# Optimization experiments

Hardware: AMD Instinct MI355X
Metric: run time of the kernel (lower is better)

## Reference

```python
import jax, jax.numpy as jnp
import numpy as np

# config constants
B, L, ENC_IN = 8, 512, 7
D_MODEL = 768
EXPAND = 2
D_INNER = D_MODEL * EXPAND          # 1536
DT_RANK = (D_MODEL + 15) // 16      # 48
N_STATE = 16                         # configs.d_ff acts as SSM state size
K_CONV = 4
E_LAYERS = 2
C_OUT = 7
PRED_LEN = 96
EPS = 1e-5


def rmsnorm(x, w):
    return x * jax.lax.rsqrt(jnp.mean(x * x, axis=-1, keepdims=True) + EPS) * w


def silu(x):
    return x * jax.nn.sigmoid(x)


def positional_embedding(l, d):
    pos = np.arange(l, dtype=np.float32)[:, None]
    div = np.exp(np.arange(0, d, 2, dtype=np.float32) * (-np.log(10000.0) / d))
    pe = np.zeros((l, d), dtype=np.float32)
    pe[:, 0::2] = np.sin(pos * div)
    pe[:, 1::2] = np.cos(pos * div)
    return jnp.asarray(pe)


def causal_dwconv(x, w, b):
    # x: [b, d, l], w: [d, 1, k]; torch pads k-1 both sides then slices [:l] == left-pad k-1
    y = jax.lax.conv_general_dilated(
        x, w, window_strides=(1,), padding=[(K_CONV - 1, 0)],
        dimension_numbers=('NCH', 'OIH', 'NCH'), feature_group_count=D_INNER)
    return y + b[None, :, None]


def selective_scan(u, delta, A, Bm, Cm, Dp):
    # u, delta: [b,l,d]; A: [d,n]; Bm, Cm: [b,l,n]; Dp: [d]
    deltaA = jnp.exp(jnp.einsum('bld,dn->bldn', delta, A))          # [b,l,d,n]
    deltaBu = (delta * u)[..., None] * Bm[:, :, None, :]             # [b,l,d,n]

    def step(xc, inp):
        dA, dBu, Ct = inp                                            # [b,d,n],[b,d,n],[b,n]
        xc = dA * xc + dBu
        return xc, jnp.einsum('bdn,bn->bd', xc, Ct)

    b, l, d = u.shape
    x0 = jnp.zeros((b, d, A.shape[1]), u.dtype)
    _, ys = jax.lax.scan(step, x0, (jnp.moveaxis(deltaA, 1, 0),
                                    jnp.moveaxis(deltaBu, 1, 0),
                                    jnp.moveaxis(Cm, 1, 0)))
    y = jnp.moveaxis(ys, 0, 1)                                       # [b,l,d]
    return y + u * Dp


def mamba_block(x, in_w, conv_w, conv_b, xproj_w, dtproj_w, dtproj_b, A_log, Dp, outproj_w):
    xr = x @ in_w.T                                                  # [b,l,2*d_inner]
    xs, res = xr[..., :D_INNER], xr[..., D_INNER:]
    xs = causal_dwconv(jnp.swapaxes(xs, 1, 2), conv_w, conv_b)
    xs = silu(jnp.swapaxes(xs, 1, 2))
    # ssm
    A = -jnp.exp(A_log)
    x_dbl = xs @ xproj_w.T                                           # [b,l,dt_rank+2n]
    delta = x_dbl[..., :DT_RANK]
    Bm = x_dbl[..., DT_RANK:DT_RANK + N_STATE]
    Cm = x_dbl[..., DT_RANK + N_STATE:]
    delta = jax.nn.softplus(delta @ dtproj_w.T + dtproj_b)
    y = selective_scan(xs, delta, A, Bm, Cm, Dp)
    y = y * silu(res)
    return y @ outproj_w.T


def setup_inputs() -> dict:
    key = jax.random.key(0)
    ks = iter(jax.random.split(key, 32))
    s = 0.02
    d = {}
    d['x'] = jax.random.normal(next(ks), (B, L, ENC_IN), jnp.float32)
    d['token_w'] = jax.random.normal(next(ks), (D_MODEL, ENC_IN, 3), jnp.float32) * s
    d['time_w'] = jax.random.normal(next(ks), (D_MODEL, 1), jnp.float32) * s
    d['norm_w'] = jnp.ones((E_LAYERS, D_MODEL), jnp.float32)
    d['in_w'] = jax.random.normal(next(ks), (E_LAYERS, 2 * D_INNER, D_MODEL), jnp.float32) * s
    d['conv_w'] = jax.random.normal(next(ks), (E_LAYERS, D_INNER, 1, K_CONV), jnp.float32) * s
    d['conv_b'] = jnp.zeros((E_LAYERS, D_INNER), jnp.float32)
    d['xproj_w'] = jax.random.normal(next(ks), (E_LAYERS, DT_RANK + 2 * N_STATE, D_INNER), jnp.float32) * s
    d['dtproj_w'] = jax.random.normal(next(ks), (E_LAYERS, D_INNER, DT_RANK), jnp.float32) * s
    d['dtproj_b'] = jnp.zeros((E_LAYERS, D_INNER), jnp.float32)
    A = np.tile(np.arange(1, N_STATE + 1, dtype=np.float32)[None, :], (D_INNER, 1))
    d['A_log'] = jnp.tile(jnp.log(jnp.asarray(A))[None], (E_LAYERS, 1, 1))
    d['Dp'] = jnp.ones((E_LAYERS, D_INNER), jnp.float32)
    d['outproj_w'] = jax.random.normal(next(ks), (E_LAYERS, D_MODEL, D_INNER), jnp.float32) * s
    d['final_norm_w'] = jnp.ones((D_MODEL,), jnp.float32)
    d['out_w'] = jax.random.normal(next(ks), (C_OUT, D_MODEL), jnp.float32) * s
    return d


def reference(x, token_w, time_w, norm_w, in_w, conv_w, conv_b, xproj_w,
              dtproj_w, dtproj_b, A_log, Dp, outproj_w, final_norm_w, out_w):
    # instance normalization (mean/std detached)
    mean_enc = jax.lax.stop_gradient(jnp.mean(x, axis=1, keepdims=True))
    xc = x - mean_enc
    std_enc = jax.lax.stop_gradient(jnp.sqrt(jnp.var(xc, axis=1, keepdims=True) + 1e-5))
    xc = xc / std_enc
    # DataEmbedding: circular conv token emb + sinusoidal pos + timeF linear
    xp = jnp.pad(jnp.swapaxes(xc, 1, 2), ((0, 0), (0, 0), (1, 1)), mode='wrap')
    tok = jax.lax.conv_general_dilated(xp, token_w, (1,), 'VALID',
                                       dimension_numbers=('NCH', 'OIH', 'NCH'))
    tok = jnp.swapaxes(tok, 1, 2)                                    # [b,l,d_model]
    x_mark = (jnp.arange(L, dtype=x.dtype) / L)[None, :, None]       # [1,l,1]
    h = tok + positional_embedding(L, D_MODEL)[None] + x_mark @ time_w.T
    for e in range(E_LAYERS):
        h = mamba_block(rmsnorm(h, norm_w[e]), in_w[e], conv_w[e], conv_b[e],
                        xproj_w[e], dtproj_w[e], dtproj_b[e], A_log[e], Dp[e],
                        outproj_w[e]) + h
    h = rmsnorm(h, final_norm_w)
    out = h @ out_w.T
    out = out * std_enc + mean_enc
    return out[:, -PRED_LEN:, :]
```

## Files before the change

### kernel.cpp

```cpp
#include <hip/hip_runtime.h>
#include <hip/hip_bf16.h>
#include <math.h>

#define BSZ 8
#define LSEQ 512
#define ENC_IN 7
#define D_MODEL 768
#define D_INNER 1536
#define DT_RANK 48
#define N_STATE 16
#define K_CONV 4
#define E_LAYERS 2
#define C_OUT 7
#define PRED_LEN 96
#define EPSV 1e-5f
#define XN 80
#define KSPLIT 4

#define ROWS (BSZ*LSEQ)
#define NC 16
#define CL (LSEQ/NC)
#define NTILE (LSEQ/16)
#define LOG2E 1.44269504088896f

typedef __bf16 bf16x8 __attribute__((ext_vector_type(8)));
typedef float  f32x4  __attribute__((ext_vector_type(4)));

__device__ __forceinline__ float fexp2(float x) {
    float r;
    asm("v_exp_f32 %0, %1" : "=v"(r) : "v"(x));
    return r;
}
__device__ __forceinline__ float softplusf(float v) {
    return fmaxf(v, 0.f) + log1pf(__expf(-fabsf(v)));
}
__device__ __forceinline__ void glds16(const char* g, char* l) {
    __builtin_amdgcn_global_load_lds((const __attribute__((address_space(1))) unsigned int*)g,
                                     (__attribute__((address_space(3))) unsigned int*)l, 16, 0, 0);
}

__device__ __forceinline__ float block_sum(float v, float* tmp) {
    #pragma unroll
    for (int off = 32; off > 0; off >>= 1) v += __shfl_down(v, off);
    int lane = threadIdx.x & 63, wid = threadIdx.x >> 6;
    __syncthreads();
    if (lane == 0) tmp[wid] = v;
    __syncthreads();
    return tmp[0] + tmp[1] + tmp[2] + tmp[3];
}

__global__ __launch_bounds__(256) void cvt_all(const float* __restrict__ in_w,
                                               const float* __restrict__ outw,
                                               const float* __restrict__ xpw,
                                               const float* __restrict__ dtw,
                                               __hip_bfloat16* __restrict__ inw_bf,
                                               __hip_bfloat16* __restrict__ outw_bf,
                                               __hip_bfloat16* __restrict__ xpw_bf,
                                               __hip_bfloat16* __restrict__ dtw_bf) {
    const int N1 = E_LAYERS*2*D_INNER*D_MODEL;
    const int N2 = E_LAYERS*D_MODEL*D_INNER;
    const int N3 = E_LAYERS*XN*D_INNER;
    const int N4 = E_LAYERS*D_INNER*64;
    int i = blockIdx.x*256 + threadIdx.x;
    if (i < N1) {
        inw_bf[i] = __float2bfloat16(in_w[i]);
    } else if (i < N1+N2) {
        int j = i - N1; outw_bf[j] = __float2bfloat16(outw[j]);
    } else if (i < N1+N2+N3) {
        int j = i - N1 - N2; xpw_bf[j] = __float2bfloat16(xpw[j]);
    } else if (i < N1+N2+N3+N4) {
        int j = i - N1 - N2 - N3;
        int r = j >> 6, c = j & 63;
        dtw_bf[j] = __float2bfloat16(c < DT_RANK ? dtw[r*DT_RANK + c] : 0.f);
    }
}

__global__ __launch_bounds__(256) void stats_kernel(const float* __restrict__ x,
                                                    float* __restrict__ mean,
                                                    float* __restrict__ stdv) {
    int bc = blockIdx.x;
    int b = bc / ENC_IN, c = bc % ENC_IN;
    __shared__ float tmp[4];
    float s = 0.f, sq = 0.f;
    for (int l = threadIdx.x; l < LSEQ; l += 256) {
        float v = x[((size_t)(b*LSEQ + l))*ENC_IN + c];
        s += v; sq += v*v;
    }
    s = block_sum(s, tmp);
    sq = block_sum(sq, tmp);
    if (threadIdx.x == 0) {
        float m = s / LSEQ;
        float var = sq / LSEQ - m*m;
        if (var < 0.f) var = 0.f;
        mean[bc] = m;
        stdv[bc] = sqrtf(var + EPSV);
    }
}

__global__ __launch_bounds__(256) void embed_kernel(const float* __restrict__ x,
                                                    const float* __restrict__ token_w,
                                                    const float* __restrict__ time_w,
                                                    const float* __restrict__ mean,
                                                    const float* __restrict__ stdv,
                                                    float* __restrict__ h) {
    int bl = blockIdx.x;
    int b = bl >> 9, l = bl & 511;
    __shared__ float sxc[ENC_IN*3];
    if (threadIdx.x < ENC_IN*3) {
        int c = threadIdx.x / 3, k = threadIdx.x % 3;
        int lk = (l + k - 1) & 511;
        float v = x[((size_t)(b*LSEQ + lk))*ENC_IN + c];
        sxc[threadIdx.x] = (v - mean[b*ENC_IN + c]) / stdv[b*ENC_IN + c];
    }
    __syncthreads();
    #pragma unroll
    for (int i = 0; i < 3; i++) {
        int d = threadIdx.x + i*256;
        float acc = 0.f;
        const float* w = token_w + (size_t)d*21;
        #pragma unroll
        for (int t = 0; t < 21; t++) acc += sxc[t] * w[t];
        int d2 = d & ~1;
        float div = __expf((float)d2 * (-9.210340371976184f / (float)D_MODEL));
        float ang = (float)l * div;
        float pe = (d & 1) ? cosf(ang) : sinf(ang);
        float tm = ((float)l / (float)LSEQ) * time_w[d];
        h[(size_t)bl*D_MODEL + d] = acc + pe + tm;
    }
}

__global__ __launch_bounds__(256) void rmsnorm_bf16(const float* __restrict__ h,
                                                    const float* __restrict__ w,
                                                    __hip_bfloat16* __restrict__ xn) {
    size_t base = (size_t)blockIdx.x * D_MODEL;
    __shared__ float tmp[4];
    float ss = 0.f;
    for (int k = threadIdx.x; k < D_MODEL; k += 256) { float v = h[base+k]; ss += v*v; }
    ss = block_sum(ss, tmp);
    float inv = rsqrtf(ss / (float)D_MODEL + EPSV);
    for (int k = threadIdx.x; k < D_MODEL; k += 256)
        xn[base+k] = __float2bfloat16(h[base+k]*inv*w[k]);
}

__global__ __launch_bounds__(256) void gemm_inproj(const __hip_bfloat16* __restrict__ A,
                                                   const __hip_bfloat16* __restrict__ Bw,
                                                   __hip_bfloat16* __restrict__ Cxs,
                                                   __hip_bfloat16* __restrict__ Cg) {
    __shared__ __align__(16) __hip_bfloat16 As[2][128*32];
    __shared__ __align__(16) __hip_bfloat16 Bs[2][128*32];
    const int K = D_MODEL;
    int tid = threadIdx.x, lane = tid & 63, w = tid >> 6;
    int gx = gridDim.x;
    int nwg = gx * gridDim.y;
    int orig = blockIdx.y*gx + blockIdx.x;
    int swz = (orig & 7)*(nwg >> 3) + (orig >> 3);
    int m0 = (swz / gx) * 128, n0 = (swz % gx) * 128;
    int wr = w >> 1, wc = w & 1;
    int kq = lane >> 4, rr = lane & 15;

    f32x4 acc[4][4];
    #pragma unroll
    for (int i = 0; i < 4; i++)
        #pragma unroll
        for (int j = 0; j < 4; j++) acc[i][j] = (f32x4){0.f,0.f,0.f,0.f};

    const char* Ab = (const char*)A;
    const char* Bb = (const char*)Bw;
    char* AsB = (char*)As;
    char* BsB = (char*)Bs;

    int c0 = tid, c1 = tid + 256;
    int r0 = c0 >> 2, q0 = (c0 & 3) ^ ((r0 >> 1) & 3);
    int r1 = c1 >> 2, q1 = (c1 & 3) ^ ((r1 >> 1) & 3);
    int sw = (kq ^ ((rr >> 1) & 3)) * 16;

    glds16(Ab + ((size_t)(m0+r0)*K + 0 + q0*8)*2, AsB + c0*16);
    glds16(Ab + ((size_t)(m0+r1)*K + 0 + q1*8)*2, AsB + c1*16);
    glds16(Bb + ((size_t)(n0+r0)*K + 0 + q0*8)*2, BsB + c0*16);
    glds16(Bb + ((size_t)(n0+r1)*K + 0 + q1*8)*2, BsB + c1*16);
    asm volatile("s_waitcnt vmcnt(0)" ::: "memory");
    __syncthreads();

    int cur = 0;
    for (int k0 = 0; k0 < K; k0 += 32) {
        if (k0 + 32 < K) {
            int nb = cur ^ 1;
            glds16(Ab + ((size_t)(m0+r0)*K + k0+32 + q0*8)*2, AsB + nb*8192 + c0*16);
            glds16(Ab + ((size_t)(m0+r1)*K + k0+32 + q1*8)*2, AsB + nb*8192 + c1*16);
            glds16(Bb + ((size_t)(n0+r0)*K + k0+32 + q0*8)*2, BsB + nb*8192 + c0*16);
            glds16(Bb + ((size_t)(n0+r1)*K + k0+32 + q1*8)*2, BsB + nb*8192 + c1*16);
        }
        bf16x8 af[4], bfr[4];
        #pragma unroll
        for (int mi = 0; mi < 4; mi++) af[mi]  = *(const bf16x8*)(AsB + cur*8192 + (wr*64 + mi*16 + rr)*64 + sw);
        #pragma unroll
        for (int ni = 0; ni < 4; ni++) bfr[ni] = *(const bf16x8*)(BsB + cur*8192 + (wc*64 + ni*16 + rr)*64 + sw);
        #pragma unroll
        for (int mi = 0; mi < 4; mi++)
            #pragma unroll
            for (int ni = 0; ni < 4; ni++)
                acc[mi][ni] = __builtin_amdgcn_mfma_f32_16x16x32_bf16(af[mi], bfr[ni], acc[mi][ni], 0, 0, 0);
        asm volatile("s_waitcnt vmcnt(0)" ::: "memory");
        __syncthreads();
        cur ^= 1;
    }

    #pragma unroll
    for (int mi = 0; mi < 4; mi++) {
        #pragma unroll
        for (int ni = 0; ni < 4; ni++) {
            int row0 = m0 + wr*64 + mi*16;
            int col  = n0 + wc*64 + ni*16 + rr;
            if (col >= D_INNER) {
                __hip_bfloat16 g4[4];
                #pragma unroll
                for (int r = 0; r < 4; r++) {
                    float v = acc[mi][ni][r];
                    g4[r] = __float2bfloat16(v / (1.f + __expf(-v)));
                }
                int cd = col - D_INNER;
                *(uint2*)&Cg[((size_t)(row0 >> 4)*D_INNER + cd)*16 + kq*4] = *(uint2*)g4;
            } else {
                #pragma unroll
                for (int r = 0; r < 4; r++) {
                    int row = row0 + kq*4 + r;
                    Cxs[(size_t)row*D_INNER + col] = __float2bfloat16(acc[mi][ni][r]);
                }
            }
        }
    }
}

__global__ __launch_bounds__(256) void gemm_dtproj(const __hip_bfloat16* __restrict__ A,
                                                   const __hip_bfloat16* __restrict__ Bw,
                                                   const float* __restrict__ bias,
                                                   __hip_bfloat16* __restrict__ C) {
    __shared__ __align__(16) __hip_bfloat16 As[128*64];
    __shared__ __align__(16) __hip_bfloat16 Bs[128*64];
    const int K = 64;
    int tid = threadIdx.x, lane = tid & 63, w = tid >> 6;
    int gx = gridDim.x;
    int nwg = gx * gridDim.y;
    int orig = blockIdx.y*gx + blockIdx.x;
    int swz = (orig & 7)*(nwg >> 3) + (orig >> 3);
    int m0 = (swz / gx) * 128, n0 = (swz % gx) * 128;
    int wr = w >> 1, wc = w & 1;
    int kq = lane >> 4, rr = lane & 15;

    f32x4 acc[4][4];
    #pragma unroll
    for (int i = 0; i < 4; i++)
        #pragma unroll
        for (int j = 0; j < 4; j++) acc[i][j] = (f32x4){0.f,0.f,0.f,0.f};

    const char* Ab = (const char*)A;
    const char* Bb = (const char*)Bw;
    char* AsB = (char*)As;
    char* BsB = (char*)Bs;

    #pragma unroll
    for (int c = 0; c < 4; c++) {
        int idx = c*256 + tid;
        int r = idx >> 3, q = idx & 7;
        int qs = q ^ (r & 7);
        glds16(Ab + ((size_t)(m0+r)*K + qs*8)*2, AsB + idx*16);
        glds16(Bb + ((size_t)(n0+r)*K + qs*8)*2, BsB + idx*16);
    }
    __syncthreads();

    #pragma unroll
    for (int kh = 0; kh < 2; kh++) {
        int ch = ((kh*4 + kq) ^ (rr & 7)) * 16;
        bf16x8 af[4], bfr[4];
        #pragma unroll
        for (int mi = 0; mi < 4; mi++) af[mi]  = *(const bf16x8*)(AsB + (wr*64 + mi*16 + rr)*128 + ch);
        #pragma unroll
        for (int ni = 0; ni < 4; ni++) bfr[ni] = *(const bf16x8*)(BsB + (wc*64 + ni*16 + rr)*128 + ch);
        #pragma unroll
        for (int mi = 0; mi < 4; mi++)
            #pragma unroll
            for (int ni = 0; ni < 4; ni++)
                acc[mi][ni] = __builtin_amdgcn_mfma_f32_16x16x32_bf16(af[mi], bfr[ni], acc[mi][ni], 0, 0, 0);
    }

    #pragma unroll
    for (int mi = 0; mi < 4; mi++) {
        #pragma unroll
        for (int ni = 0; ni < 4; ni++) {
            int row0 = m0 + wr*64 + mi*16;
            int col  = n0 + wc*64 + ni*16 + rr;
            __hip_bfloat16 d4[4];
            #pragma unroll
            for (int r = 0; r < 4; r++) {
                float v = acc[mi][ni][r] + bias[col];
                d4[r] = __float2bfloat16(softplusf(v));
            }
            *(uint2*)&C[((size_t)(row0 >> 4)*D_INNER + col)*16 + kq*4] = *(uint2*)d4;
        }
    }
}

__global__ __launch_bounds__(256) void gemm_outproj(const __hip_bfloat16* __restrict__ A,
                                                    const __hip_bfloat16* __restrict__ Bw,
                                                    float* __restrict__ C) {
    __shared__ __align__(16) __hip_bfloat16 As[2][128*32];
    __shared__ __align__(16) __hip_bfloat16 Bs[2][64*32];
    int tid = threadIdx.x, lane = tid & 63, w = tid >> 6;
    int gx = gridDim.x;
    int nwg = gx * gridDim.y;
    int orig = blockIdx.y*gx + blockIdx.x;
    int swz = (orig & 7)*(nwg >> 3) + (orig >> 3);
    int m0 = (swz / gx) * 128, n0 = (swz % gx) * 64;
    int wr = w >> 1, wc = w & 1;
    int kq = lane >> 4, rr = lane & 15;
    const int K = D_INNER;

    f32x4 acc[4][2];
    #pragma unroll
    for (int i = 0; i < 4; i++)
        #pragma unroll
        for (int j = 0; j < 2; j++) acc[i][j] = (f32x4){0.f,0.f,0.f,0.f};

    const char* Ab = (const char*)A;
    const char* Bb = (const char*)Bw;
    char* AsB = (char*)As;
    char* BsB = (char*)Bs;

    int cA0 = tid, cA1 = tid + 256;
    int rA0 = cA0 >> 2, qA0 = (cA0 & 3) ^ ((rA0 >> 1) & 3);
    int rA1 = cA1 >> 2, qA1 = (cA1 & 3) ^ ((rA1 >> 1) & 3);
    int rB = tid >> 2,  qB  = (tid & 3) ^ ((rB >> 1) & 3);
    int sw = (kq ^ ((rr >> 1) & 3)) * 16;

    glds16(Ab + ((size_t)(m0+rA0)*K + 0 + qA0*8)*2, AsB + cA0*16);
    glds16(Ab + ((size_t)(m0+rA1)*K + 0 + qA1*8)*2, AsB + cA1*16);
    glds16(Bb + ((size_t)(n0+rB)*K + 0 + qB*8)*2, BsB + tid*16);
    asm volatile("s_waitcnt vmcnt(0)" ::: "memory");
    __syncthreads();

    int cur = 0;
    for (int k0 = 0; k0 < K; k0 += 32) {
        if (k0 + 32 < K) {
            int nb = cur ^ 1;
            glds16(Ab + ((size_t)(m0+rA0)*K + k0+32 + qA0*8)*2, AsB + nb*8192 + cA0*16);
            glds16(Ab + ((size_t)(m0+rA1)*K + k0+32 + qA1*8)*2, AsB + nb*8192 + cA1*16);
            glds16(Bb + ((size_t)(n0+rB)*K + k0+32 + qB*8)*2, BsB + nb*4096 + tid*16);
        }
        bf16x8 af[4], bfr[2];
        #pragma unroll
        for (int mi = 0; mi < 4; mi++) af[mi]  = *(const bf16x8*)(AsB + cur*8192 + (wr*64 + mi*16 + rr)*64 + sw);
        #pragma unroll
        for (int ni = 0; ni < 2; ni++) bfr[ni] = *(const bf16x8*)(BsB + cur*4096 + (wc*32 + ni*16 + rr)*64 + sw);
        #pragma unroll
        for (int mi = 0; mi < 4; mi++)
            #pragma unroll
            for (int ni = 0; ni < 2; ni++)
                acc[mi][ni] = __builtin_amdgcn_mfma_f32_16x16x32_bf16(af[mi], bfr[ni], acc[mi][ni], 0, 0, 0);
        asm volatile("s_waitcnt vmcnt(0)" ::: "memory");
        __syncthreads();
        cur ^= 1;
    }

    #pragma unroll
    for (int mi = 0; mi < 4; mi++) {
        #pragma unroll
        for (int ni = 0; ni < 2; ni++) {
            #pragma unroll
            for (int r = 0; r < 4; r++) {
                int row = m0 + wr*64 + mi*16 + kq*4 + r;
                int col = n0 + wc*32 + ni*16 + rr;
                size_t o = (size_t)row*D_MODEL + col;
                C[o] = acc[mi][ni][r] + C[o];
            }
        }
    }
}

__global__ __launch_bounds__(256) void gemm_xproj(const __hip_bfloat16* __restrict__ A,
                                                  const __hip_bfloat16* __restrict__ W,
                                                  float* __restrict__ P) {
    __shared__ __align__(16) __hip_bfloat16 As[2][64*64];
    __shared__ __align__(16) __hip_bfloat16 Bs[2][96*64];
    int tid = threadIdx.x, lane = tid & 63, w = tid >> 6;
    int m0 = blockIdx.x * 64;
    int k0 = blockIdx.y * (D_INNER / KSPLIT);
    int kq = lane >> 4, rr = lane & 15;
    f32x4 acc[5];
    #pragma unroll
    for (int i = 0; i < 5; i++) acc[i] = (f32x4){0.f,0.f,0.f,0.f};
    const char* Ab = (const char*)A;
    const char* Wb = (const char*)W;
    char* AsB = (char*)As;
    char* BsB = (char*)Bs;

    auto stageA = [&](int buf, int kk) {
        #pragma unroll
        for (int cA = 0; cA < 2; cA++) {
            int idx = cA*256 + tid;
            int r = idx >> 3, q = (idx & 7) ^ (r & 7);
            glds16(Ab + ((size_t)(m0+r)*D_INNER + kk + q*8)*2, AsB + buf*8192 + idx*16);
        }
        #pragma unroll
        for (int cB = 0; cB < 3; cB++) {
            int idx = cB*256 + tid;
            int r = idx >> 3, q = (idx & 7) ^ (r & 7);
            int rs = r < XN ? r : XN-1;
            glds16(Wb + ((size_t)rs*D_INNER + kk + q*8)*2, BsB + buf*12288 + idx*16);
        }
    };

    stageA(0, k0);
    asm volatile("s_waitcnt vmcnt(0)" ::: "memory");
    __syncthreads();

    int cur = 0;
    const int kend = k0 + D_INNER/KSPLIT;
    for (int kk = k0; kk < kend; kk += 64) {
        if (kk + 64 < kend) stageA(cur ^ 1, kk + 64);
        #pragma unroll
        for (int kh = 0; kh < 2; kh++) {
            bf16x8 a = *(const bf16x8*)(AsB + cur*8192 + (w*16 + rr)*128 + (((kh*4 + kq) ^ (rr & 7)))*16);
            #pragma unroll
            for (int ni = 0; ni < 5; ni++) {
                bf16x8 b = *(const bf16x8*)(BsB + cur*12288 + (ni*16 + rr)*128 + (((kh*4 + kq) ^ (rr & 7)))*16);
                acc[ni] = __builtin_amdgcn_mfma_f32_16x16x32_bf16(a, b, acc[ni], 0, 0, 0);
            }
        }
        asm volatile("s_waitcnt vmcnt(0)" ::: "memory");
        __syncthreads();
        cur ^= 1;
    }
    float* Cp = P + (size_t)blockIdx.y * ROWS * XN;
    #pragma unroll
    for (int ni = 0; ni < 5; ni++)
        #pragma unroll
        for (int r = 0; r < 4; r++) {
            int row = m0 + w*16 + kq*4 + r;
            int col = ni*16 + rr;
            Cp[(size_t)row*XN + col] = acc[ni][r];
        }
}

__global__ __launch_bounds__(256) void xproj_reduce(const float* __restrict__ P,
                                                    float* __restrict__ xdbl,
                                                    __hip_bfloat16* __restrict__ xdbl_bf) {
    int idx = blockIdx.x*256 + threadIdx.x;
    int col = idx % 96, row = idx / 96;
    if (row >= ROWS) return;
    const size_t RX = (size_t)ROWS*XN;
    if (col < XN) {
        size_t o = (size_t)row*XN + col;
        float s = P[o] + P[RX + o] + P[2*RX + o] + P[3*RX + o];
        xdbl[o] = s;
        if (col < DT_RANK) xdbl_bf[(size_t)row*64 + col] = __float2bfloat16(s);
    } else {
        xdbl_bf[(size_t)row*64 + col - 32] = __float2bfloat16(0.f);
    }
}

__global__ __launch_bounds__(256) void dwconv_silu(const __hip_bfloat16* __restrict__ xs,
                                                   const float* __restrict__ cw,
                                                   const float* __restrict__ cb,
                                                   __hip_bfloat16* __restrict__ u_bf) {
    int idx = blockIdx.x*256 + threadIdx.x;
    int dg = idx % (D_INNER/8);
    int t  = idx / (D_INNER/8);
    if (t >= ROWS) return;
    int d0 = dg*8;
    int l = t & 511, b = t >> 9;
    bf16x8 rows[K_CONV];
    #pragma unroll
    for (int k = 0; k < K_CONV; k++) {
        int ll = l - (K_CONV-1) + k;
        if (ll >= 0) rows[k] = *(const bf16x8*)(xs + ((size_t)(b*LSEQ + ll))*D_INNER + d0);
        else { bf16x8 z = {}; rows[k] = z; }
    }
    bf16x8 outv;
    #pragma unroll
    for (int j = 0; j < 8; j++) {
        int d = d0 + j;
        const float4 w4 = *(const float4*)(cw + d*K_CONV);
        float acc = cb[d]
                  + (float)rows[0][j]*w4.x + (float)rows[1][j]*w4.y
                  + (float)rows[2][j]*w4.z + (float)rows[3][j]*w4.w;
        float v = acc / (1.f + __expf(-acc));
        outv[j] = (__bf16)v;
    }
    *(bf16x8*)(u_bf + (size_t)t*D_INNER + d0) = outv;
}

__global__ __launch_bounds__(256) void scan_p1(const __hip_bfloat16* __restrict__ u,
                                               const __hip_bfloat16* __restrict__ delta_blk,
                                               const float* __restrict__ xdbl,
                                               const float* __restrict__ A_log,
                                               float* __restrict__ xfin,
                                               float* __restrict__ sumdlt) {
    int d = blockIdx.x*256 + threadIdx.x;
    int c = blockIdx.y, b = blockIdx.z;
    int l0 = c*CL;
    const float* al = A_log + d*N_STATE;
    bool fast = true;
    #pragma unroll
    for (int n = 0; n < N_STATE; n++)
        fast = fast && (fabsf(__expf(al[n]) - (float)(n+1)) < 1e-3f);
    float xs[N_STATE];
    #pragma unroll
    for (int n = 0; n < N_STATE; n++) xs[n] = 0.f;
    const __hip_bfloat16* pu = u + (size_t)(b*LSEQ + l0)*D_INNER + d;
    const float* pB = xdbl + (size_t)(b*LSEQ + l0)*XN + DT_RANK;
    float sd = 0.f;
    if (fast) {
        #pragma unroll
        for (int tt = 0; tt < 2; tt++) {
            const __hip_bfloat16* db = delta_blk + ((size_t)(b*NTILE + (l0>>4) + tt)*D_INNER + d)*16;
            bf16x8 d0 = *(const bf16x8*)db;
            bf16x8 d1 = *(const bf16x8*)(db + 8);
            #pragma unroll
            for (int i = 0; i < 16; i++) {
                float dlt = (float)(i < 8 ? d0[i] : d1[i-8]);
                float uu = __bfloat162float(*pu); pu += D_INNER;
                float du = dlt*uu;
                sd += dlt;
                float e1 = fexp2(-dlt*LOG2E);
                float e = e1;
                xs[0] = e*xs[0] + du*pB[0];
                #pragma unroll
                for (int n = 1; n < N_STATE; n++) {
                    e *= e1;
                    xs[n] = e*xs[n] + du*pB[n];
                }
                pB += XN;
            }
        }
    } else {
        #pragma unroll
        for (int tt = 0; tt < 2; tt++) {
            const __hip_bfloat16* db = delta_blk + ((size_t)(b*NTILE + (l0>>4) + tt)*D_INNER + d)*16;
            bf16x8 d0 = *(const bf16x8*)db;
            bf16x8 d1 = *(const bf16x8*)(db + 8);
            #pragma unroll
            for (int i = 0; i < 16; i++) {
                float dlt = (float)(i < 8 ? d0[i] : d1[i-8]);
                float uu = __bfloat162float(*pu); pu += D_INNER;
                float du = dlt*uu;
                sd += dlt;
                #pragma unroll
                for (int n = 0; n < N_STATE; n++) {
                    float A2n = -__expf(al[n]) * LOG2E;
                    xs[n] = fexp2(dlt*A2n)*xs[n] + du*pB[n];
                }
                pB += XN;
            }
        }
    }
    float* px = xfin + (size_t)((b*NC + c)*N_STATE)*D_INNER + d;
    #pragma unroll
    for (int n = 0; n < N_STATE; n++) px[n*D_INNER] = xs[n];
    sumdlt[(size_t)(b*NC + c)*D_INNER + d] = sd;
}

__global__ __launch_bounds__(256) void scan_p2(float* __restrict__ xfin,
                                               const float* __restrict__ sumdlt,
                                               const float* __restrict__ A_log) {
    int idx = blockIdx.x*256 + threadIdx.x;
    int d = idx % D_INNER;
    int r = idx / D_INNER;
    int n = r & 15;
    int b = r >> 4;
    float A2 = -__expf(A_log[d*N_STATE + n]) * LOG2E;
    float cr = 0.f;
    for (int c = 1; c < NC; c++) {
        size_t jp = (size_t)(b*NC + c - 1);
        float xf = xfin[(jp*N_STATE + n)*D_INNER + d];
        float s  = sumdlt[jp*D_INNER + d];
        cr = fexp2(A2 * s) * cr + xf;
        xfin[(jp*N_STATE + n)*D_INNER + d] = cr;
    }
}

__global__ __launch_bounds__(256) void scan_p3(const __hip_bfloat16* __restrict__ u,
                                               const __hip_bfloat16* __restrict__ delta_blk,
                                               const __hip_bfloat16* __restrict__ gres,
                                               const float* __restrict__ xdbl,
                                               const float* __restrict__ A_log,
                                               const float* __restrict__ Dp,
                                               const float* __restrict__ carry,
                                               __hip_bfloat16* __restrict__ ygate) {
    int d = blockIdx.x*256 + threadIdx.x;
    int c = blockIdx.y, b = blockIdx.z;
    int l0 = c*CL;
    const float* al = A_log + d*N_STATE;
    bool fast = true;
    #pragma unroll
    for (int n = 0; n < N_STATE; n++)
        fast = fast && (fabsf(__expf(al[n]) - (float)(n+1)) < 1e-3f);
    float xs[N_STATE];
    if (c == 0) {
        #pragma unroll
        for (int n = 0; n < N_STATE; n++) xs[n] = 0.f;
    } else {
        const float* pc = carry + (size_t)((b*NC + c - 1)*N_STATE)*D_INNER + d;
        #pragma unroll
        for (int n = 0; n < N_STATE; n++) xs[n] = pc[n*D_INNER];
    }
    float Dv = Dp[d];
    const __hip_bfloat16* pu = u + (size_t)(b*LSEQ + l0)*D_INNER + d;
    const float* pB = xdbl + (size_t)(b*LSEQ + l0)*XN + DT_RANK;
    __hip_bfloat16* py = ygate + (size_t)(b*LSEQ + l0)*D_INNER + d;
    if (fast) {
        #pragma unroll
        for (int tt = 0; tt < 2; tt++) {
            size_t tb = (size_t)(b*NTILE + (l0>>4) + tt)*D_INNER + d;
            const __hip_bfloat16* db = delta_blk + tb*16;
            bf16x8 d0 = *(const bf16x8*)db;
            bf16x8 d1 = *(const bf16x8*)(db + 8);
            const __hip_bfloat16* gb = gres + tb*16;
            bf16x8 g0 = *(const bf16x8*)gb;
            bf16x8 g1 = *(const bf16x8*)(gb + 8);
            #pragma unroll
            for (int i = 0; i < 16; i++) {
                float dlt = (float)(i < 8 ? d0[i] : d1[i-8]);
                float gr  = (float)(i < 8 ? g0[i] : g1[i-8]);
                float uu = __bfloat162float(*pu); pu += D_INNER;
                float du = dlt*uu;
                float e1 = fexp2(-dlt*LOG2E);
                float e = e1;
                float acc;
                xs[0] = e*xs[0] + du*pB[0];
                acc = xs[0]*pB[N_STATE + 0];
                #pragma unroll
                for (int n = 1; n < N_STATE; n++) {
                    e *= e1;
                    xs[n] = e*xs[n] + du*pB[n];
                    acc += xs[n]*pB[N_STATE + n];
                }
                pB += XN;
                float y = acc + uu*Dv;
                *py = __float2bfloat16(y * gr); py += D_INNER;
            }
        }
    } else {
        #pragma unroll
        for (int tt = 0; tt < 2; tt++) {
            size_t tb = (size_t)(b*NTILE + (l0>>4) + tt)*D_INNER + d;
            const __hip_bfloat16* db = delta_blk + tb*16;
            bf16x8 d0 = *(const bf16x8*)db;
            bf16x8 d1 = *(const bf16x8*)(db + 8);
            const __hip_bfloat16* gb = gres + tb*16;
            bf16x8 g0 = *(const bf16x8*)gb;
            bf16x8 g1 = *(const bf16x8*)(gb + 8);
            #pragma unroll
            for (int i = 0; i < 16; i++) {
                float dlt = (float)(i < 8 ? d0[i] : d1[i-8]);
                float gr  = (float)(i < 8 ? g0[i] : g1[i-8]);
                float uu = __bfloat162float(*pu); pu += D_INNER;
                float du = dlt*uu;
                float acc = 0.f;
                #pragma unroll
                for (int n = 0; n < N_STATE; n++) {
                    float A2n = -__expf(al[n]) * LOG2E;
                    xs[n] = fexp2(dlt*A2n)*xs[n] + du*pB[n];
                    acc += xs[n]*pB[N_STATE + n];
                }
                pB += XN;
                float y = acc + uu*Dv;
                *py = __float2bfloat16(y * gr); py += D_INNER;
            }
        }
    }
}

__global__ __launch_bounds__(256) void final_kernel(const float* __restrict__ h,
                                                    const float* __restrict__ fnw,
                                                    const float* __restrict__ out_w,
                                                    const float* __restrict__ mean,
                                                    const float* __restrict__ stdv,
                                                    float* __restrict__ out) {
    int bid = blockIdx.x;
    int b = bid / PRED_LEN, lo = bid % PRED_LEN;
    int l = LSEQ - PRED_LEN + lo;
    const float* row = h + ((size_t)(b*LSEQ + l))*D_MODEL;
    __shared__ float tmp[4];
    float ss = 0.f;
    for (int k = threadIdx.x; k < D_MODEL; k += 256) { float v = row[k]; ss += v*v; }
    ss = block_sum(ss, tmp);
    float inv = rsqrtf(ss / (float)D_MODEL + EPSV);
    float acc[C_OUT] = {};
    for (int k = threadIdx.x; k < D_MODEL; k += 256) {
        float hn = row[k]*fnw[k];
        #pragma unroll
        for (int c = 0; c < C_OUT; c++) acc[c] += hn*out_w[c*D_MODEL + k];
    }
    #pragma unroll
    for (int c = 0; c < C_OUT; c++) {
        float s = block_sum(acc[c], tmp);
        if (threadIdx.x == 0)
            out[((size_t)(b*PRED_LEN + lo))*C_OUT + c] = s*inv*stdv[b*ENC_IN + c] + mean[b*ENC_IN + c];
    }
}

extern "C" void kernel_launch(void* const* d_in, const int* in_sizes, int n_in,
                              void* d_out, int out_size, void* d_ws, size_t ws_size,
                              hipStream_t stream) {
    const float* x        = (const float*)d_in[0];
    const float* token_w  = (const float*)d_in[1];
    const float* time_w   = (const float*)d_in[2];
    const float* norm_w   = (const float*)d_in[3];
    const float* in_w     = (const float*)d_in[4];
    const float* conv_w   = (const float*)d_in[5];
    const float* conv_b   = (const float*)d_in[6];
    const float* xproj_w  = (const float*)d_in[7];
    const float* dtproj_w = (const float*)d_in[8];
    const float* dtproj_b = (const float*)d_in[9];
    const float* A_log    = (const float*)d_in[10];
    const float* Dp       = (const float*)d_in[11];
    const float* outproj_w= (const float*)d_in[12];
    const float* final_nw = (const float*)d_in[13];
    const float* out_w    = (const float*)d_in[14];
    float* out = (float*)d_out;

    float* ws   = (float*)d_ws;
    float* mean = ws;
    float* stdv = ws + 64;
    float* h    = ws + 128;
    float* xdbl = h    + (size_t)ROWS*D_MODEL;
    float* sumd = xdbl + (size_t)ROWS*XN;
    float* xfin = sumd + (size_t)BSZ*NC*D_INNER;
    float* pout = xfin + (size_t)BSZ*NC*D_INNER*N_STATE;
    float* fend = pout + (size_t)KSPLIT*ROWS*XN;
    __hip_bfloat16* xn_bf  = (__hip_bfloat16*)fend;
    __hip_bfloat16* xs_bf  = xn_bf + (size_t)ROWS*D_MODEL;
    __hip_bfloat16* u_bf   = xs_bf + (size_t)ROWS*D_INNER;
    __hip_bfloat16* gres   = u_bf  + (size_t)ROWS*D_INNER;
    __hip_bfloat16* ygate  = gres  + (size_t)ROWS*D_INNER;
    __hip_bfloat16* delta  = ygate + (size_t)ROWS*D_INNER;
    __hip_bfloat16* xdbl_bf= delta + (size_t)ROWS*D_INNER;
    __hip_bfloat16* inw_bf = xdbl_bf+ (size_t)ROWS*64;
    __hip_bfloat16* outw_bf= inw_bf + (size_t)E_LAYERS*2*D_INNER*D_MODEL;
    __hip_bfloat16* xpw_bf = outw_bf+ (size_t)E_LAYERS*D_MODEL*D_INNER;
    __hip_bfloat16* dtw_bf = xpw_bf + (size_t)E_LAYERS*XN*D_INNER;

    {
        const int NT = E_LAYERS*2*D_INNER*D_MODEL + E_LAYERS*D_MODEL*D_INNER
                     + E_LAYERS*XN*D_INNER + E_LAYERS*D_INNER*64;
        cvt_all<<<(NT+255)/256, 256, 0, stream>>>(in_w, outproj_w, xproj_w, dtproj_w,
                                                  inw_bf, outw_bf, xpw_bf, dtw_bf);
    }

    stats_kernel<<<BSZ*ENC_IN, 256, 0, stream>>>(x, mean, stdv);
    embed_kernel<<<ROWS, 256, 0, stream>>>(x, token_w, time_w, mean, stdv, h);

    for (int e = 0; e < E_LAYERS; e++) {
        rmsnorm_bf16<<<ROWS, 256, 0, stream>>>(h, norm_w + e*D_MODEL, xn_bf);
        gemm_inproj<<<dim3(2*D_INNER/128, ROWS/128), 256, 0, stream>>>(
            xn_bf, inw_bf + (size_t)e*2*D_INNER*D_MODEL, xs_bf, gres);
        dwconv_silu<<<(ROWS*(D_INNER/8) + 255)/256, 256, 0, stream>>>(
            xs_bf, conv_w + (size_t)e*D_INNER*K_CONV, conv_b + e*D_INNER, u_bf);
        gemm_xproj<<<dim3(ROWS/64, KSPLIT), 256, 0, stream>>>(
            u_bf, xpw_bf + (size_t)e*XN*D_INNER, pout);
        xproj_reduce<<<(ROWS*96 + 255)/256, 256, 0, stream>>>(pout, xdbl, xdbl_bf);
        gemm_dtproj<<<dim3(D_INNER/128, ROWS/128), 256, 0, stream>>>(
            xdbl_bf, dtw_bf + (size_t)e*D_INNER*64, dtproj_b + e*D_INNER, delta);
        const float* Alog_e = A_log + (size_t)e*D_INNER*N_STATE;
        scan_p1<<<dim3(D_INNER/256, NC, BSZ), 256, 0, stream>>>(
            u_bf, delta, xdbl, Alog_e, xfin, sumd);
        scan_p2<<<(BSZ*D_INNER*N_STATE)/256, 256, 0, stream>>>(
            xfin, sumd, Alog_e);
        scan_p3<<<dim3(D_INNER/256, NC, BSZ), 256, 0, stream>>>(
            u_bf, delta, gres, xdbl, Alog_e, Dp + (size_t)e*D_INNER, xfin, ygate);
        gemm_outproj<<<dim3(D_MODEL/64, ROWS/128), 256, 0, stream>>>(
            ygate, outw_bf + (size_t)e*D_MODEL*D_INNER, h);
    }

    final_kernel<<<BSZ*PRED_LEN, 256, 0, stream>>>(h, final_nw, out_w, mean, stdv, out);
}
```

Measured before the change: 387.3 us.

## Triple-buffer GEMM k-loops and fuse x_proj split-K reduction into dt_proj

The in_proj, out_proj and x_proj GEMMs move from double to triple-buffered LDS staging. They prefetch two tiles ahead and use partial vmcnt waits plus raw barriers, so global loads overlap with MFMA work and no longer drain every iteration. The separate xproj_reduce kernel is removed. gemm_dtproj now sums the four split-K partials itself, writes the fp32 xdbl from the n0==0 blocks, and builds the bf16 A tile directly in LDS. This saves a launch and a round trip through memory, but every dt_proj block redoes the partial-sum reads, and the larger LDS footprint may reduce occupancy.

```diff
diff --git a/kernel.cpp b/kernel.cpp
--- a/kernel.cpp
+++ b/kernel.cpp
@@ -146,9 +146,10 @@
                                                    const __hip_bfloat16* __restrict__ Bw,
                                                    __hip_bfloat16* __restrict__ Cxs,
                                                    __hip_bfloat16* __restrict__ Cg) {
-    __shared__ __align__(16) __hip_bfloat16 As[2][128*32];
-    __shared__ __align__(16) __hip_bfloat16 Bs[2][128*32];
+    __shared__ __align__(16) __hip_bfloat16 As[3][128*32];
+    __shared__ __align__(16) __hip_bfloat16 Bs[3][128*32];
     const int K = D_MODEL;
+    const int NK = K/32;
     int tid = threadIdx.x, lane = tid & 63, w = tid >> 6;
     int gx = gridDim.x;
     int nwg = gx * gridDim.y;
@@ -174,22 +175,23 @@
     int r1 = c1 >> 2, q1 = (c1 & 3) ^ ((r1 >> 1) & 3);
     int sw = (kq ^ ((rr >> 1) & 3)) * 16;
 
-    glds16(Ab + ((size_t)(m0+r0)*K + 0 + q0*8)*2, AsB + c0*16);
-    glds16(Ab + ((size_t)(m0+r1)*K + 0 + q1*8)*2, AsB + c1*16);
-    glds16(Bb + ((size_t)(n0+r0)*K + 0 + q0*8)*2, BsB + c0*16);
-    glds16(Bb + ((size_t)(n0+r1)*K + 0 + q1*8)*2, BsB + c1*16);
-    asm volatile("s_waitcnt vmcnt(0)" ::: "memory");
-    __syncthreads();
-
-    int cur = 0;
-    for (int k0 = 0; k0 < K; k0 += 32) {
-        if (k0 + 32 < K) {
-            int nb = cur ^ 1;
-            glds16(Ab + ((size_t)(m0+r0)*K + k0+32 + q0*8)*2, AsB + nb*8192 + c0*16);
-            glds16(Ab + ((size_t)(m0+r1)*K + k0+32 + q1*8)*2, AsB + nb*8192 + c1*16);
-            glds16(Bb + ((size_t)(n0+r0)*K + k0+32 + q0*8)*2, BsB + nb*8192 + c0*16);
-            glds16(Bb + ((size_t)(n0+r1)*K + k0+32 + q1*8)*2, BsB + nb*8192 + c1*16);
-        }
+    auto stage = [&](int buf, int kt) {
+        int k0 = kt*32;
+        glds16(Ab + ((size_t)(m0+r0)*K + k0 + q0*8)*2, AsB + buf*8192 + c0*16);
+        glds16(Ab + ((size_t)(m0+r1)*K + k0 + q1*8)*2, AsB + buf*8192 + c1*16);
+        glds16(Bb + ((size_t)(n0+r0)*K + k0 + q0*8)*2, BsB + buf*8192 + c0*16);
+        glds16(Bb + ((size_t)(n0+r1)*K + k0 + q1*8)*2, BsB + buf*8192 + c1*16);
+    };
+
+    stage(0, 0);
+    stage(1, 1);
+
+    for (int k = 0; k < NK; k++) {
+        int cur = k % 3;
+        __builtin_amdgcn_s_barrier();
+        if (k + 2 < NK) stage((k + 2) % 3, k + 2);
+        asm volatile("s_waitcnt vmcnt(8)" ::: "memory");
+        __builtin_amdgcn_s_barrier();
         bf16x8 af[4], bfr[4];
         #pragma unroll
         for (int mi = 0; mi < 4; mi++) af[mi]  = *(const bf16x8*)(AsB + cur*8192 + (wr*64 + mi*16 + rr)*64 + sw);
@@ -200,9 +202,6 @@
             #pragma unroll
             for (int ni = 0; ni < 4; ni++)
                 acc[mi][ni] = __builtin_amdgcn_mfma_f32_16x16x32_bf16(af[mi], bfr[ni], acc[mi][ni], 0, 0, 0);
-        asm volatile("s_waitcnt vmcnt(0)" ::: "memory");
-        __syncthreads();
-        cur ^= 1;
     }
 
     #pragma unroll
@@ -231,10 +230,11 @@
     }
 }
 
-__global__ __launch_bounds__(256) void gemm_dtproj(const __hip_bfloat16* __restrict__ A,
+__global__ __launch_bounds__(256) void gemm_dtproj(const float* __restrict__ P,
                                                    const __hip_bfloat16* __restrict__ Bw,
                                                    const float* __restrict__ bias,
-                                                   __hip_bfloat16* __restrict__ C) {
+                                                   float* __restrict__ xdbl,
+                                                   __hip_bfloat16* __restrict__ delta) {
     __shared__ __align__(16) __hip_bfloat16 As[128*64];
     __shared__ __align__(16) __hip_bfloat16 Bs[128*64];
     const int K = 64;
@@ -253,7 +253,6 @@
         #pragma unroll
         for (int j = 0; j < 4; j++) acc[i][j] = (f32x4){0.f,0.f,0.f,0.f};
 
-    const char* Ab = (const char*)A;
     const char* Bb = (const char*)Bw;
     char* AsB = (char*)As;
     char* BsB = (char*)Bs;
@@ -263,8 +262,36 @@
         int idx = c*256 + tid;
         int r = idx >> 3, q = idx & 7;
         int qs = q ^ (r & 7);
-        glds16(Ab + ((size_t)(m0+r)*K + qs*8)*2, AsB + idx*16);
         glds16(Bb + ((size_t)(n0+r)*K + qs*8)*2, BsB + idx*16);
+    }
+
+    const size_t RX = (size_t)ROWS*XN;
+    #pragma unroll
+    for (int it = 0; it < 2; it++) {
+        int idx = it*1024 + tid;
+        if (idx < 128*10) {
+            int row = idx / 10, ch = idx % 10;
+            const float* p0 = P + (size_t)(m0+row)*XN + ch*8;
+            f32x4 a0 = *(const f32x4*)(p0)      + *(const f32x4*)(p0+RX)
+                     + *(const f32x4*)(p0+2*RX) + *(const f32x4*)(p0+3*RX);
+            f32x4 a1 = *(const f32x4*)(p0+4)        + *(const f32x4*)(p0+RX+4)
+                     + *(const f32x4*)(p0+2*RX+4)   + *(const f32x4*)(p0+3*RX+4);
+            if (n0 == 0) {
+                float* xd = xdbl + (size_t)(m0+row)*XN + ch*8;
+                *(f32x4*)(xd)   = a0;
+                *(f32x4*)(xd+4) = a1;
+            }
+            if (ch < 8) {
+                bf16x8 hv;
+                if (ch < 6) {
+                    #pragma unroll
+                    for (int j = 0; j < 4; j++) { hv[j] = (__bf16)a0[j]; hv[4+j] = (__bf16)a1[j]; }
+                } else {
+                    bf16x8 z = {}; hv = z;
+                }
+                *(bf16x8*)(AsB + row*128 + ((ch ^ (row & 7))*16)) = hv;
+            }
+        }
     }
     __syncthreads();
 
@@ -295,7 +322,7 @@
                 float v = acc[mi][ni][r] + bias[col];
                 d4[r] = __float2bfloat16(softplusf(v));
             }
-            *(uint2*)&C[((size_t)(row0 >> 4)*D_INNER + col)*16 + kq*4] = *(uint2*)d4;
+            *(uint2*)&delta[((size_t)(row0 >> 4)*D_INNER + col)*16 + kq*4] = *(uint2*)d4;
         }
     }
 }
@@ -303,8 +330,8 @@
 __global__ __launch_bounds__(256) void gemm_outproj(const __hip_bfloat16* __restrict__ A,
                                                     const __hip_bfloat16* __restrict__ Bw,
                                                     float* __restrict__ C) {
-    __shared__ __align__(16) __hip_bfloat16 As[2][128*32];
-    __shared__ __align__(16) __hip_bfloat16 Bs[2][64*32];
+    __shared__ __align__(16) __hip_bfloat16 As[3][128*32];
+    __shared__ __align__(16) __hip_bfloat16 Bs[3][64*32];
     int tid = threadIdx.x, lane = tid & 63, w = tid >> 6;
     int gx = gridDim.x;
     int nwg = gx * gridDim.y;
@@ -314,6 +341,7 @@
     int wr = w >> 1, wc = w & 1;
     int kq = lane >> 4, rr = lane & 15;
     const int K = D_INNER;
+    const int NK = K/32;
 
     f32x4 acc[4][2];
     #pragma unroll
@@ -332,20 +360,22 @@
     int rB = tid >> 2,  qB  = (tid & 3) ^ ((rB >> 1) & 3);
     int sw = (kq ^ ((rr >> 1) & 3)) * 16;
 
-    glds16(Ab + ((size_t)(m0+rA0)*K + 0 + qA0*8)*2, AsB + cA0*16);
-    glds16(Ab + ((size_t)(m0+rA1)*K + 0 + qA1*8)*2, AsB + cA1*16);
-    glds16(Bb + ((size_t)(n0+rB)*K + 0 + qB*8)*2, BsB + tid*16);
-    asm volatile("s_waitcnt vmcnt(0)" ::: "memory");
-    __syncthreads();
-
-    int cur = 0;
-    for (int k0 = 0; k0 < K; k0 += 32) {
-        if (k0 + 32 < K) {
-            int nb = cur ^ 1;
-            glds16(Ab + ((size_t)(m0+rA0)*K + k0+32 + qA0*8)*2, AsB + nb*8192 + cA0*16);
-            glds16(Ab + ((size_t)(m0+rA1)*K + k0+32 + qA1*8)*2, AsB + nb*8192 + cA1*16);
-            glds16(Bb + ((size_t)(n0+rB)*K + k0+32 + qB*8)*2, BsB + nb*4096 + tid*16);
-        }
+    auto stage = [&](int buf, int kt) {
+        int k0 = kt*32;
+        glds16(Ab + ((size_t)(m0+rA0)*K + k0 + qA0*8)*2, AsB + buf*8192 + cA0*16);
+        glds16(Ab + ((size_t)(m0+rA1)*K + k0 + qA1*8)*2, AsB + buf*8192 + cA1*16);
+        glds16(Bb + ((size_t)(n0+rB)*K + k0 + qB*8)*2,  BsB + buf*4096 + tid*16);
+    };
+
+    stage(0, 0);
+    stage(1, 1);
+
+    for (int k = 0; k < NK; k++) {
+        int cur = k % 3;
+        __builtin_amdgcn_s_barrier();
+        if (k + 2 < NK) stage((k + 2) % 3, k + 2);
+        asm volatile("s_waitcnt vmcnt(6)" ::: "memory");
+        __builtin_amdgcn_s_barrier();
         bf16x8 af[4], bfr[2];
         #pragma unroll
         for (int mi = 0; mi < 4; mi++) af[mi]  = *(const bf16x8*)(AsB + cur*8192 + (wr*64 + mi*16 + rr)*64 + sw);
@@ -356,9 +386,6 @@
             #pragma unroll
             for (int ni = 0; ni < 2; ni++)
                 acc[mi][ni] = __builtin_amdgcn_mfma_f32_16x16x32_bf16(af[mi], bfr[ni], acc[mi][ni], 0, 0, 0);
-        asm volatile("s_waitcnt vmcnt(0)" ::: "memory");
-        __syncthreads();
-        cur ^= 1;
     }
 
     #pragma unroll
@@ -379,12 +406,13 @@
 __global__ __launch_bounds__(256) void gemm_xproj(const __hip_bfloat16* __restrict__ A,
                                                   const __hip_bfloat16* __restrict__ W,
                                                   float* __restrict__ P) {
-    __shared__ __align__(16) __hip_bfloat16 As[2][64*64];
-    __shared__ __align__(16) __hip_bfloat16 Bs[2][96*64];
+    __shared__ __align__(16) __hip_bfloat16 As[3][64*64];
+    __shared__ __align__(16) __hip_bfloat16 Bs[3][96*64];
     int tid = threadIdx.x, lane = tid & 63, w = tid >> 6;
     int m0 = blockIdx.x * 64;
     int k0 = blockIdx.y * (D_INNER / KSPLIT);
     int kq = lane >> 4, rr = lane & 15;
+    const int NK = (D_INNER/KSPLIT)/64;
     f32x4 acc[5];
     #pragma unroll
     for (int i = 0; i < 5; i++) acc[i] = (f32x4){0.f,0.f,0.f,0.f};
@@ -393,7 +421,8 @@
     char* AsB = (char*)As;
     char* BsB = (char*)Bs;
 
-    auto stageA = [&](int buf, int kk) {
+    auto stage = [&](int buf, int it) {
+        int kk = k0 + it*64;
         #pragma unroll
         for (int cA = 0; cA < 2; cA++) {
             int idx = cA*256 + tid;
@@ -409,14 +438,15 @@
         }
     };
 
-    stageA(0, k0);
-    asm volatile("s_waitcnt vmcnt(0)" ::: "memory");
-    __syncthreads();
-
-    int cur = 0;
-    const int kend = k0 + D_INNER/KSPLIT;
-    for (int kk = k0; kk < kend; kk += 64) {
-        if (kk + 64 < kend) stageA(cur ^ 1, kk + 64);
+    stage(0, 0);
+    stage(1, 1);
+
+    for (int it = 0; it < NK; it++) {
+        int cur = it % 3;
+        __builtin_amdgcn_s_barrier();
+        if (it + 2 < NK) stage((it + 2) % 3, it + 2);
+        asm volatile("s_waitcnt vmcnt(10)" ::: "memory");
+        __builtin_amdgcn_s_barrier();
         #pragma unroll
         for (int kh = 0; kh < 2; kh++) {
             bf16x8 a = *(const bf16x8*)(AsB + cur*8192 + (w*16 + rr)*128 + (((kh*4 + kq) ^ (rr & 7)))*16);
@@ -426,9 +456,6 @@
                 acc[ni] = __builtin_amdgcn_mfma_f32_16x16x32_bf16(a, b, acc[ni], 0, 0, 0);
             }
         }
-        asm volatile("s_waitcnt vmcnt(0)" ::: "memory");
-        __syncthreads();
-        cur ^= 1;
     }
     float* Cp = P + (size_t)blockIdx.y * ROWS * XN;
     #pragma unroll
@@ -439,23 +466,6 @@
             int col = ni*16 + rr;
             Cp[(size_t)row*XN + col] = acc[ni][r];
         }
-}
-
-__global__ __launch_bounds__(256) void xproj_reduce(const float* __restrict__ P,
-                                                    float* __restrict__ xdbl,
-                                                    __hip_bfloat16* __restrict__ xdbl_bf) {
-    int idx = blockIdx.x*256 + threadIdx.x;
-    int col = idx % 96, row = idx / 96;
-    if (row >= ROWS) return;
-    const size_t RX = (size_t)ROWS*XN;
-    if (col < XN) {
-        size_t o = (size_t)row*XN + col;
-        float s = P[o] + P[RX + o] + P[2*RX + o] + P[3*RX + o];
-        xdbl[o] = s;
-        if (col < DT_RANK) xdbl_bf[(size_t)row*64 + col] = __float2bfloat16(s);
-    } else {
-        xdbl_bf[(size_t)row*64 + col - 32] = __float2bfloat16(0.f);
-    }
 }
 
 __global__ __launch_bounds__(256) void dwconv_silu(const __hip_bfloat16* __restrict__ xs,
@@ -734,8 +744,7 @@
     __hip_bfloat16* gres   = u_bf  + (size_t)ROWS*D_INNER;
     __hip_bfloat16* ygate  = gres  + (size_t)ROWS*D_INNER;
     __hip_bfloat16* delta  = ygate + (size_t)ROWS*D_INNER;
-    __hip_bfloat16* xdbl_bf= delta + (size_t)ROWS*D_INNER;
-    __hip_bfloat16* inw_bf = xdbl_bf+ (size_t)ROWS*64;
+    __hip_bfloat16* inw_bf = delta + (size_t)ROWS*D_INNER;
     __hip_bfloat16* outw_bf= inw_bf + (size_t)E_LAYERS*2*D_INNER*D_MODEL;
     __hip_bfloat16* xpw_bf = outw_bf+ (size_t)E_LAYERS*D_MODEL*D_INNER;
     __hip_bfloat16* dtw_bf = xpw_bf + (size_t)E_LAYERS*XN*D_INNER;
@@ -758,9 +767,8 @@
             xs_bf, conv_w + (size_t)e*D_INNER*K_CONV, conv_b + e*D_INNER, u_bf);
         gemm_xproj<<<dim3(ROWS/64, KSPLIT), 256, 0, stream>>>(
             u_bf, xpw_bf + (size_t)e*XN*D_INNER, pout);
-        xproj_reduce<<<(ROWS*96 + 255)/256, 256, 0, stream>>>(pout, xdbl, xdbl_bf);
         gemm_dtproj<<<dim3(D_INNER/128, ROWS/128), 256, 0, stream>>>(
-            xdbl_bf, dtw_bf + (size_t)e*D_INNER*64, dtproj_b + e*D_INNER, delta);
+            pout, dtw_bf + (size_t)e*D_INNER*64, dtproj_b + e*D_INNER, xdbl, delta);
         const float* Alog_e = A_log + (size_t)e*D_INNER*N_STATE;
         scan_p1<<<dim3(D_INNER/256, NC, BSZ), 256, 0, stream>>>(
             u_bf, delta, xdbl, Alog_e, xfin, sumd);
```

Result: faster. 376.4 us (-2.8%).
